# Performance work log

Measured on AMD Instinct MI355X. Metric: run time of the kernel, lower is better.

The kernel has to match this reference:

```python
import jax, jax.numpy as jnp
import numpy as np

B, T, R = 64, 32, 49          # batch, seq_len, num image regions
E = 512                        # embed_size == hidden_size
L = 2                          # num_layers
V = 30000                      # vocab_size


def setup_inputs() -> dict:
    key = jax.random.key(0)
    ks = jax.random.split(key, 8)
    s = 1.0 / np.sqrt(E)  # xavier-ish scale for recurrent weights
    return {
        "features": jax.random.normal(ks[0], (B, R, E), jnp.float32),
        "captions": jax.random.randint(ks[1], (B, T), 0, V),
        "embed_table": jax.random.normal(ks[2], (V, E), jnp.float32) * 0.01,
        "W_ih": jax.random.normal(ks[3], (L, 4 * E, E), jnp.float32) * s,
        "W_hh": jax.random.normal(ks[4], (L, 4 * E, E), jnp.float32) * s,
        "b_ih": jnp.zeros((L, 4 * E), jnp.float32),
        "b_hh": jnp.zeros((L, 4 * E), jnp.float32),
        "W_lin": jax.random.normal(ks[5], (V, 2 * E), jnp.float32) * 0.01,
        "b_lin": jnp.zeros((V,), jnp.float32),
    }


def reference(features, captions, embed_table, W_ih, W_hh, b_ih, b_hh, W_lin, b_lin):
    num_layers = W_ih.shape[0]
    emb = embed_table[captions]                        # [B, T, E]
    mean_f = features.mean(axis=1)                     # [B, E]
    h0 = jnp.stack([mean_f] * num_layers)              # [L, B, H]
    c0 = jnp.stack([mean_f] * num_layers)

    def step(carry, x_t):
        h, c = carry                                   # each [L, B, H]
        inp = x_t                                      # [B, E]
        hs, cs = [], []
        for l in range(num_layers):
            gates = inp @ W_ih[l].T + b_ih[l] + h[l] @ W_hh[l].T + b_hh[l]
            i, f, g, o = jnp.split(gates, 4, axis=-1)  # PyTorch gate order i,f,g,o
            c_new = jax.nn.sigmoid(f) * c[l] + jax.nn.sigmoid(i) * jnp.tanh(g)
            h_new = jax.nn.sigmoid(o) * jnp.tanh(c_new)
            hs.append(h_new)
            cs.append(c_new)
            inp = h_new
        h_top = inp                                    # [B, H]
        # dot attention over image regions
        scores = jnp.einsum('brd,bd->br', features, h_top)
        alpha = jax.nn.softmax(scores, axis=1)
        context = jnp.einsum('br,brd->bd', alpha, features)
        logit = jnp.concatenate([h_top, context], axis=1) @ W_lin.T + b_lin
        return (jnp.stack(hs), jnp.stack(cs)), logit

    _, logits = jax.lax.scan(step, (h0, c0), jnp.swapaxes(emb, 0, 1))  # [T, B, V]
    return jnp.swapaxes(logits, 0, 1)                  # [B, T, V]
```

## Files before the change

### kernel.cpp

```cpp
#include <hip/hip_runtime.h>

#define B_ 64
#define T_ 32
#define R_ 49
#define E_ 512
#define V_ 30000

using bfrag = __attribute__((ext_vector_type(8))) short;
using ffrag = __attribute__((ext_vector_type(4))) float;

__device__ __forceinline__ float bf2f(short u) {
    union { unsigned u32; float f; } x;
    x.u32 = ((unsigned)(unsigned short)u) << 16;
    return x.f;
}
__device__ __forceinline__ unsigned short f2bf(float f) {
    union { float f; unsigned u; } x; x.f = f;
    unsigned r = x.u + 0x7fffu + ((x.u >> 16) & 1u);
    return (unsigned short)(r >> 16);
}
__device__ __forceinline__ float sigm(float x) { return 1.f / (1.f + __expf(-x)); }

#define GLDS(g, l) __builtin_amdgcn_global_load_lds( \
    (const __attribute__((address_space(1))) void*)(g), \
    (__attribute__((address_space(3))) void*)(l), 16, 0, 0)

__global__ __launch_bounds__(256)
void cvt_kernel(const float* __restrict__ src, unsigned short* __restrict__ dst, int n8)
{
    int i = blockIdx.x * 256 + threadIdx.x;
    if (i >= n8) return;
    const float4* s = (const float4*)src + (size_t)i * 2;
    float4 a = s[0], b = s[1];
    bfrag o;
    o[0] = (short)f2bf(a.x); o[1] = (short)f2bf(a.y);
    o[2] = (short)f2bf(a.z); o[3] = (short)f2bf(a.w);
    o[4] = (short)f2bf(b.x); o[5] = (short)f2bf(b.y);
    o[6] = (short)f2bf(b.z); o[7] = (short)f2bf(b.w);
    *(bfrag*)(dst + (size_t)i * 8) = o;
}

__global__ __launch_bounds__(256)
void gemm_bt(const unsigned short* __restrict__ A,
             const unsigned short* __restrict__ W,
             const float* __restrict__ bias1,
             const float* __restrict__ bias2,
             float* __restrict__ outp,
             int M, int N, int K)
{
    __shared__ __align__(16) unsigned short As[128 * 32];
    __shared__ __align__(16) unsigned short Bs[128 * 32];
    const int tid  = threadIdx.x;
    const int wave = tid >> 6, lane = tid & 63;
    const int lrow = lane & 15, kq = lane >> 4;

    const int gx = gridDim.x;
    const int nwg = gx * gridDim.y;
    int bid = blockIdx.y * gx + blockIdx.x;
    if ((nwg & 7) == 0) {
        const int cpx = nwg >> 3;
        bid = (bid & 7) * cpx + (bid >> 3);
    }
    const int m0 = (bid % gx) * 128, n0 = (bid / gx) * 128;

    const int wm = (wave >> 1) * 64, wn = (wave & 1) * 64;

    ffrag acc[4][4];
#pragma unroll
    for (int i = 0; i < 4; i++)
#pragma unroll
        for (int j = 0; j < 4; j++) acc[i][j] = ffrag{0.f, 0.f, 0.f, 0.f};

    const int ca = tid, cb = 256 + tid;
    const int ar0 = m0 + (ca >> 2), ar1 = m0 + (cb >> 2);
    const int k8a = (ca & 3) * 8, k8b = (cb & 3) * 8;
    const int wr0 = min(n0 + (ca >> 2), N - 1);
    const int wr1 = min(n0 + (cb >> 2), N - 1);

    unsigned short* ldsA0 = As + (wave * 64) * 8;
    unsigned short* ldsA1 = As + (256 + wave * 64) * 8;
    unsigned short* ldsB0 = Bs + (wave * 64) * 8;
    unsigned short* ldsB1 = Bs + (256 + wave * 64) * 8;

    for (int k0 = 0; k0 < K; k0 += 32) {
        GLDS(A + (size_t)ar0 * K + k0 + k8a, ldsA0);
        GLDS(A + (size_t)ar1 * K + k0 + k8b, ldsA1);
        GLDS(W + (size_t)wr0 * K + k0 + k8a, ldsB0);
        GLDS(W + (size_t)wr1 * K + k0 + k8b, ldsB1);
        __syncthreads();
        bfrag af[4], bw[4];
#pragma unroll
        for (int i = 0; i < 4; i++)
            af[i] = *(const bfrag*)(As + (wm + i * 16 + lrow) * 32 + kq * 8);
#pragma unroll
        for (int j = 0; j < 4; j++)
            bw[j] = *(const bfrag*)(Bs + (wn + j * 16 + lrow) * 32 + kq * 8);
#pragma unroll
        for (int i = 0; i < 4; i++)
#pragma unroll
            for (int j = 0; j < 4; j++)
                acc[i][j] = __builtin_amdgcn_mfma_f32_16x16x32_bf16(af[i], bw[j], acc[i][j], 0, 0, 0);
        __syncthreads();
    }

#pragma unroll
    for (int j = 0; j < 4; j++) {
        int col  = n0 + wn + j * 16 + lrow;
        int colc = min(col, N - 1);
        float bs = 0.f;
        if (bias1) bs += bias1[colc];
        if (bias2) bs += bias2[colc];
        bool ok = (col < N);
#pragma unroll
        for (int i = 0; i < 4; i++) {
            int rbase = m0 + wm + i * 16 + kq * 4;
#pragma unroll
            for (int r = 0; r < 4; r++) {
                float v = acc[i][j][r] + bs;
                if (ok) outp[(size_t)(rbase + r) * N + col] = v;
            }
        }
    }
}

__global__ __launch_bounds__(256)
void lstm_step(const unsigned short* __restrict__ Wbih,
               const unsigned short* __restrict__ Wbhh,
               const float* __restrict__ X0,
               const float* __restrict__ b_ih,
               const float* __restrict__ b_hh,
               unsigned short* __restrict__ H0,
               unsigned short* __restrict__ Htop,
               float* __restrict__ c0, float* __restrict__ c1,
               int t1, int t2)
{
    const int layer = blockIdx.x >> 7;
    const int blk   = blockIdx.x & 127;
    const int tid  = threadIdx.x;
    const int wave = tid >> 6, lane = tid & 63;
    const int lrow = lane & 15, kq = lane >> 4;
    const int b0 = (blk & 3) * 16;
    const int e0 = (blk >> 2) * 16;
    const int wr = wave * 512 + e0 + lrow;
    const size_t BE = (size_t)B_ * E_;

    const unsigned short *xin, *hprev, *Wih, *Whh;
    const float *pre, *bih, *bhh;
    unsigned short* hout; float* cst;

    if (layer == 0) {
        if (t1 < 0) return;
        xin = nullptr; Wih = nullptr;
        Whh = Wbhh;
        pre = X0 + (size_t)t1 * B_ * 2048;
        bih = nullptr; bhh = nullptr;
        hprev = H0 + (size_t)t1 * BE;
        hout  = H0 + (size_t)(t1 + 1) * BE;
        cst = c0;
    } else {
        if (t2 < 0) return;
        xin = H0 + (size_t)(t2 + 1) * BE;
        Wih = Wbih + 2048 * 512;
        Whh = Wbhh + 2048 * 512;
        pre = nullptr;
        bih = b_ih + 2048; bhh = b_hh + 2048;
        hprev = Htop + (size_t)t2 * BE;
        hout  = Htop + (size_t)(t2 + 1) * BE;
        cst = c1;
    }

    ffrag acc = {0.f, 0.f, 0.f, 0.f};
    if (xin) {
#pragma unroll
        for (int k0 = 0; k0 < 512; k0 += 32) {
            bfrag a = *(const bfrag*)(xin + (b0 + lrow) * 512 + k0 + kq * 8);
            bfrag w = *(const bfrag*)(Wih + (size_t)wr * 512 + k0 + kq * 8);
            acc = __builtin_amdgcn_mfma_f32_16x16x32_bf16(a, w, acc, 0, 0, 0);
        }
    }
#pragma unroll
    for (int k0 = 0; k0 < 512; k0 += 32) {
        bfrag a = *(const bfrag*)(hprev + (b0 + lrow) * 512 + k0 + kq * 8);
        bfrag w = *(const bfrag*)(Whh + (size_t)wr * 512 + k0 + kq * 8);
        acc = __builtin_amdgcn_mfma_f32_16x16x32_bf16(a, w, acc, 0, 0, 0);
    }

    __shared__ float gb[4][16][17];
#pragma unroll
    for (int r = 0; r < 4; r++) gb[wave][kq * 4 + r][lrow] = acc[r];
    __syncthreads();

    const int m = tid >> 4, el = tid & 15;
    const int b = b0 + m, e = e0 + el;
    float gi = gb[0][m][el], gf = gb[1][m][el], gg = gb[2][m][el], go = gb[3][m][el];
    if (pre) {
        const float* p = pre + (size_t)b * 2048;
        gi += p[e]; gf += p[512 + e]; gg += p[1024 + e]; go += p[1536 + e];
    }
    if (bih) {
        gi += bih[e]        + bhh[e];
        gf += bih[512 + e]  + bhh[512 + e];
        gg += bih[1024 + e] + bhh[1024 + e];
        go += bih[1536 + e] + bhh[1536 + e];
    }
    float cold = cst[(size_t)b * 512 + e];
    float cn = sigm(gf) * cold + sigm(gi) * tanhf(gg);
    float hn = sigm(go) * tanhf(cn);
    cst[(size_t)b * 512 + e]  = cn;
    hout[(size_t)b * 512 + e] = f2bf(hn);
}

__global__ __launch_bounds__(256)
void attn_kernel(const float* __restrict__ features,
                 const unsigned short* __restrict__ Htop,
                 unsigned short* __restrict__ Z)
{
    const int bt = blockIdx.x;
    const int b = bt >> 5, t = bt & 31;
    const unsigned short* h = Htop + ((size_t)(t + 1) * B_ + b) * E_;
    const float* f = features + (size_t)b * R_ * E_;
    const int tid = threadIdx.x, wave = tid >> 6, lane = tid & 63;

    __shared__ float hf[E_];
    __shared__ float sc[64];
    hf[tid]       = bf2f((short)h[tid]);
    hf[256 + tid] = bf2f((short)h[256 + tid]);
    __syncthreads();

    for (int r = wave; r < R_; r += 4) {
        const float4* fr = (const float4*)(f + r * E_ + lane * 8);
        float4 v0 = fr[0], v1 = fr[1];
        const float* hp = hf + lane * 8;
        float s = v0.x * hp[0] + v0.y * hp[1] + v0.z * hp[2] + v0.w * hp[3]
                + v1.x * hp[4] + v1.y * hp[5] + v1.z * hp[6] + v1.w * hp[7];
        for (int off = 32; off; off >>= 1) s += __shfl_down(s, off);
        if (lane == 0) sc[r] = s;
    }
    __syncthreads();
    if (tid < 64) {
        float v = (tid < R_) ? sc[tid] : -3.4e38f;
        float mx = v;
        for (int off = 32; off; off >>= 1) mx = fmaxf(mx, __shfl_xor(mx, off));
        float ex = (tid < R_) ? __expf(v - mx) : 0.f;
        float sum = ex;
        for (int off = 32; off; off >>= 1) sum += __shfl_xor(sum, off);
        if (tid < R_) sc[tid] = ex / sum;
    }
    __syncthreads();

    const int e0 = tid * 2;
    float c0 = 0.f, c1 = 0.f;
    for (int r = 0; r < R_; r++) {
        float a = sc[r];
        c0 += a * f[r * E_ + e0];
        c1 += a * f[r * E_ + e0 + 1];
    }
    unsigned short* zr = Z + (size_t)bt * (2 * E_);
    zr[e0] = h[e0]; zr[e0 + 1] = h[e0 + 1];
    zr[E_ + e0]     = f2bf(c0);
    zr[E_ + e0 + 1] = f2bf(c1);
}

__global__ __launch_bounds__(256)
void init_kernel(const float* __restrict__ features,
                 const int* __restrict__ captions,
                 const float* __restrict__ embed,
                 float* __restrict__ c0, float* __restrict__ c1,
                 unsigned short* __restrict__ H0, unsigned short* __restrict__ Htop,
                 unsigned short* __restrict__ Aemb)
{
    const int blk = blockIdx.x, tid = threadIdx.x;
    if (blk < 128) {
        int g = blk * 256 + tid;
        int b = g >> 9, e = g & 511;
        float s = 0.f;
        for (int r = 0; r < R_; r++) s += features[((size_t)b * R_ + r) * E_ + e];
        float mean = s * (1.f / 49.f);
        c0[g] = mean; c1[g] = mean;
        unsigned short mb = f2bf(mean);
        H0[g] = mb; Htop[g] = mb;
    } else {
        int idx = (blk - 128) * 256 + tid;
        int row = idx >> 6, k8 = (idx & 63) * 8;
        int bb = row & 63, tt = row >> 6;
        int tok = captions[bb * T_ + tt];
        const float4* s = (const float4*)(embed + (size_t)tok * E_ + k8);
        float4 a = s[0], bq = s[1];
        bfrag o;
        o[0] = (short)f2bf(a.x);  o[1] = (short)f2bf(a.y);
        o[2] = (short)f2bf(a.z);  o[3] = (short)f2bf(a.w);
        o[4] = (short)f2bf(bq.x); o[5] = (short)f2bf(bq.y);
        o[6] = (short)f2bf(bq.z); o[7] = (short)f2bf(bq.w);
        *(bfrag*)(Aemb + (size_t)row * E_ + k8) = o;
    }
}

extern "C" void kernel_launch(void* const* d_in, const int* in_sizes, int n_in,
                              void* d_out, int out_size, void* d_ws, size_t ws_size,
                              hipStream_t stream)
{
    const float* features = (const float*)d_in[0];
    const int*   captions = (const int*)d_in[1];
    const float* embed    = (const float*)d_in[2];
    const float* W_ih     = (const float*)d_in[3];
    const float* W_hh     = (const float*)d_in[4];
    const float* b_ih     = (const float*)d_in[5];
    const float* b_hh     = (const float*)d_in[6];
    const float* W_lin    = (const float*)d_in[7];
    const float* b_lin    = (const float*)d_in[8];
    float* out = (float*)d_out;

    char* ws = (char*)d_ws;
    float*          X0     = (float*)(ws);
    unsigned short* H0     = (unsigned short*)(ws + 16777216);
    unsigned short* Htop   = (unsigned short*)(ws + 18939904);
    float*          c0     = (float*)(ws + 21102592);
    float*          c1     = (float*)(ws + 21233664);
    unsigned short* Z      = (unsigned short*)(ws + 21364736);
    unsigned short* Aemb   = (unsigned short*)(ws + 25559040);
    unsigned short* Wb_ih  = (unsigned short*)(ws + 27656192);
    unsigned short* Wb_hh  = (unsigned short*)(ws + 31850496);
    unsigned short* Wb_lin = (unsigned short*)(ws + 36044800);

    cvt_kernel<<<1024, 256, 0, stream>>>(W_ih, Wb_ih, 2 * 2048 * 512 / 8);
    cvt_kernel<<<1024, 256, 0, stream>>>(W_hh, Wb_hh, 2 * 2048 * 512 / 8);
    cvt_kernel<<<15000, 256, 0, stream>>>(W_lin, Wb_lin, V_ * 1024 / 8);

    init_kernel<<<640, 256, 0, stream>>>(features, captions, embed, c0, c1, H0, Htop, Aemb);

    gemm_bt<<<dim3(16, 16), 256, 0, stream>>>(Aemb, Wb_ih, b_ih, b_hh, X0, 2048, 2048, 512);

    for (int k = 0; k <= T_; k++) {
        lstm_step<<<256, 256, 0, stream>>>(Wb_ih, Wb_hh, X0, b_ih, b_hh,
                                           H0, Htop, c0, c1,
                                           (k < T_) ? k : -1, k - 1);
    }

    attn_kernel<<<B_ * T_, 256, 0, stream>>>(features, Htop, Z);

    gemm_bt<<<dim3(16, 235), 256, 0, stream>>>(Z, Wb_lin, b_lin, nullptr, out, 2048, V_, 1024);

    (void)in_sizes; (void)n_in; (void)out_size; (void)ws_size;
}
```

Measured before the change: 943.7 us.

## Fold attention into pipelined LSTM step launches and drop GEMM block swizzle

Removes the separate attention kernel and runs each timestep's attention in 64 extra blocks of the per-step LSTM launch, lagging two steps behind layer 0 and one behind layer 1. This adds one more launch to the wavefront pipeline. The aim is to hide attention work inside the latency-bound recurrent launches, which only use 256 blocks. It also removes the XCD-aware block-index remapping in gemm_bt, so tiles are assigned directly from blockIdx, which may hurt L2 locality on the large vocabulary GEMM.

```diff
diff --git a/kernel.cpp b/kernel.cpp
--- a/kernel.cpp
+++ b/kernel.cpp
@@ -53,16 +53,7 @@
     const int tid  = threadIdx.x;
     const int wave = tid >> 6, lane = tid & 63;
     const int lrow = lane & 15, kq = lane >> 4;
-
-    const int gx = gridDim.x;
-    const int nwg = gx * gridDim.y;
-    int bid = blockIdx.y * gx + blockIdx.x;
-    if ((nwg & 7) == 0) {
-        const int cpx = nwg >> 3;
-        bid = (bid & 7) * cpx + (bid >> 3);
-    }
-    const int m0 = (bid % gx) * 128, n0 = (bid / gx) * 128;
-
+    const int m0 = blockIdx.x * 128, n0 = blockIdx.y * 128;
     const int wm = (wave >> 1) * 64, wn = (wave & 1) * 64;
 
     ffrag acc[4][4];
@@ -132,11 +123,62 @@
                unsigned short* __restrict__ H0,
                unsigned short* __restrict__ Htop,
                float* __restrict__ c0, float* __restrict__ c1,
-               int t1, int t2)
-{
+               const float* __restrict__ features,
+               unsigned short* __restrict__ Z,
+               int t1, int t2, int ta)
+{
+    const int tid  = threadIdx.x;
+
+    if (blockIdx.x >= 256) {
+        if (ta < 0) return;
+        const int b = blockIdx.x - 256;
+        const unsigned short* h = Htop + ((size_t)(ta + 1) * B_ + b) * E_;
+        const float* f = features + (size_t)b * R_ * E_;
+        const int wave = tid >> 6, lane = tid & 63;
+
+        __shared__ float hf[E_];
+        __shared__ float sc[64];
+        hf[tid]       = bf2f((short)h[tid]);
+        hf[256 + tid] = bf2f((short)h[256 + tid]);
+        __syncthreads();
+
+        for (int r = wave; r < R_; r += 4) {
+            const float4* fr = (const float4*)(f + r * E_ + lane * 8);
+            float4 v0 = fr[0], v1 = fr[1];
+            const float* hp = hf + lane * 8;
+            float s = v0.x * hp[0] + v0.y * hp[1] + v0.z * hp[2] + v0.w * hp[3]
+                    + v1.x * hp[4] + v1.y * hp[5] + v1.z * hp[6] + v1.w * hp[7];
+            for (int off = 32; off; off >>= 1) s += __shfl_down(s, off);
+            if (lane == 0) sc[r] = s;
+        }
+        __syncthreads();
+        if (tid < 64) {
+            float v = (tid < R_) ? sc[tid] : -3.4e38f;
+            float mx = v;
+            for (int off = 32; off; off >>= 1) mx = fmaxf(mx, __shfl_xor(mx, off));
+            float ex = (tid < R_) ? __expf(v - mx) : 0.f;
+            float sum = ex;
+            for (int off = 32; off; off >>= 1) sum += __shfl_xor(sum, off);
+            if (tid < R_) sc[tid] = ex / sum;
+        }
+        __syncthreads();
+
+        const int e0 = tid * 2;
+        float cc0 = 0.f, cc1 = 0.f;
+        for (int r = 0; r < R_; r++) {
+            float a = sc[r];
+            cc0 += a * f[r * E_ + e0];
+            cc1 += a * f[r * E_ + e0 + 1];
+        }
+        unsigned short* zr = Z + (size_t)(b * T_ + ta) * (2 * E_);
+        zr[e0] = h[e0]; zr[e0 + 1] = h[e0 + 1];
+        zr[E_ + e0]     = f2bf(cc0);
+        zr[E_ + e0 + 1] = f2bf(cc1);
+        return;
+    }
+
     const int layer = blockIdx.x >> 7;
     const int blk   = blockIdx.x & 127;
-    const int tid  = threadIdx.x;
     const int wave = tid >> 6, lane = tid & 63;
     const int lrow = lane & 15, kq = lane >> 4;
     const int b0 = (blk & 3) * 16;
@@ -158,7 +200,7 @@
         hout  = H0 + (size_t)(t1 + 1) * BE;
         cst = c0;
     } else {
-        if (t2 < 0) return;
+        if (t2 < 0 || t2 >= T_) return;
         xin = H0 + (size_t)(t2 + 1) * BE;
         Wih = Wbih + 2048 * 512;
         Whh = Wbhh + 2048 * 512;
@@ -208,57 +250,6 @@
     float hn = sigm(go) * tanhf(cn);
     cst[(size_t)b * 512 + e]  = cn;
     hout[(size_t)b * 512 + e] = f2bf(hn);
-}
-
-__global__ __launch_bounds__(256)
-void attn_kernel(const float* __restrict__ features,
-                 const unsigned short* __restrict__ Htop,
-                 unsigned short* __restrict__ Z)
-{
-    const int bt = blockIdx.x;
-    const int b = bt >> 5, t = bt & 31;
-    const unsigned short* h = Htop + ((size_t)(t + 1) * B_ + b) * E_;
-    const float* f = features + (size_t)b * R_ * E_;
-    const int tid = threadIdx.x, wave = tid >> 6, lane = tid & 63;
-
-    __shared__ float hf[E_];
-    __shared__ float sc[64];
-    hf[tid]       = bf2f((short)h[tid]);
-    hf[256 + tid] = bf2f((short)h[256 + tid]);
-    __syncthreads();
-
-    for (int r = wave; r < R_; r += 4) {
-        const float4* fr = (const float4*)(f + r * E_ + lane * 8);
-        float4 v0 = fr[0], v1 = fr[1];
-        const float* hp = hf + lane * 8;
-        float s = v0.x * hp[0] + v0.y * hp[1] + v0.z * hp[2] + v0.w * hp[3]
-                + v1.x * hp[4] + v1.y * hp[5] + v1.z * hp[6] + v1.w * hp[7];
-        for (int off = 32; off; off >>= 1) s += __shfl_down(s, off);
-        if (lane == 0) sc[r] = s;
-    }
-    __syncthreads();
-    if (tid < 64) {
-        float v = (tid < R_) ? sc[tid] : -3.4e38f;
-        float mx = v;
-        for (int off = 32; off; off >>= 1) mx = fmaxf(mx, __shfl_xor(mx, off));
-        float ex = (tid < R_) ? __expf(v - mx) : 0.f;
-        float sum = ex;
-        for (int off = 32; off; off >>= 1) sum += __shfl_xor(sum, off);
-        if (tid < R_) sc[tid] = ex / sum;
-    }
-    __syncthreads();
-
-    const int e0 = tid * 2;
-    float c0 = 0.f, c1 = 0.f;
-    for (int r = 0; r < R_; r++) {
-        float a = sc[r];
-        c0 += a * f[r * E_ + e0];
-        c1 += a * f[r * E_ + e0 + 1];
-    }
-    unsigned short* zr = Z + (size_t)bt * (2 * E_);
-    zr[e0] = h[e0]; zr[e0 + 1] = h[e0 + 1];
-    zr[E_ + e0]     = f2bf(c0);
-    zr[E_ + e0 + 1] = f2bf(c1);
 }
 
 __global__ __launch_bounds__(256)
@@ -330,13 +321,12 @@
 
     gemm_bt<<<dim3(16, 16), 256, 0, stream>>>(Aemb, Wb_ih, b_ih, b_hh, X0, 2048, 2048, 512);
 
-    for (int k = 0; k <= T_; k++) {
-        lstm_step<<<256, 256, 0, stream>>>(Wb_ih, Wb_hh, X0, b_ih, b_hh,
+    for (int k = 0; k <= T_ + 1; k++) {
+        lstm_step<<<320, 256, 0, stream>>>(Wb_ih, Wb_hh, X0, b_ih, b_hh,
                                            H0, Htop, c0, c1,
-                                           (k < T_) ? k : -1, k - 1);
-    }
-
-    attn_kernel<<<B_ * T_, 256, 0, stream>>>(features, Htop, Z);
+                                           features, Z,
+                                           (k < T_) ? k : -1, k - 1, k - 2);
+    }
 
     gemm_bt<<<dim3(16, 235), 256, 0, stream>>>(Z, Wb_lin, b_lin, nullptr, out, 2048, V_, 1024);
 
```

Measured after the change: 984.1 us. 4.3% more time.
